# Optimization experiments

Measured on AMD Instinct MI355X. Metric: run time of the kernel, lower is better.

The kernel has to match this reference:

```python
import math
import jax, jax.numpy as jnp
import numpy as np

B, H, T, D = 4, 16, 1024, 64


def setup_inputs() -> dict:
    key0 = jax.random.key(0)
    ks = jax.random.split(key0, 5)
    return {
        "query": jax.random.normal(ks[0], (B, H, T, D), dtype=jnp.float32),
        "key": jax.random.normal(ks[1], (B, H, T, D), dtype=jnp.float32),
        "value": jax.random.normal(ks[2], (B, H, T, D), dtype=jnp.float32),
        "edges_key": jax.random.normal(ks[3], (T, T, D), dtype=jnp.float32),
        "edges_value": jax.random.normal(ks[4], (T, T, D), dtype=jnp.float32),
        "mask": jnp.ones((B, 1, 1, T), dtype=bool),
    }


def reference(query, key, value, edges_key, edges_value, mask):
    d = query.shape[-1]
    # content-content scores [B,H,T,T]
    scores = jnp.einsum("bhqd,bhkd->bhqk", query, key)
    # content-position scores via relative edge keys [T,T,D]
    scores = scores + jnp.einsum("bhqd,qkd->bhqk", query, edges_key)
    scores = scores * (1.0 / math.sqrt(d))
    scores = jnp.where(mask, scores, jnp.float32(-1e9))
    a = jax.nn.softmax(scores, axis=-1)  # dropout is identity in eval / pdrop=0
    # value update + relative edge-value update
    out = jnp.einsum("bhqk,bhkd->bhqd", a, value)
    out = out + jnp.einsum("bhqk,qkd->bhqd", a, edges_value)
    return out
```

## Files before the change

### kernel.cpp

```cpp
#include <hip/hip_runtime.h>

#define Tt 1024
#define Dh 64
#define BHn 64
#define SCALE 0.125f

typedef __attribute__((ext_vector_type(4))) float f32x4;
typedef __attribute__((ext_vector_type(8))) short bf16x8;

__device__ inline unsigned short f2bf(float x){
  unsigned u = __float_as_uint(x);
  unsigned r = (u + 0x7FFFu + ((u >> 16) & 1u)) >> 16;
  return (unsigned short)r;
}
__device__ inline float bf2f(unsigned short h){
  return __uint_as_float(((unsigned)h) << 16);
}
__device__ inline ushort4 pack4(float4 f){
  ushort4 u; u.x=f2bf(f.x); u.y=f2bf(f.y); u.z=f2bf(f.z); u.w=f2bf(f.w); return u;
}
__device__ inline bf16x8 pack8(float4 a, float4 b){
  bf16x8 r;
  r[0]=(short)f2bf(a.x); r[1]=(short)f2bf(a.y); r[2]=(short)f2bf(a.z); r[3]=(short)f2bf(a.w);
  r[4]=(short)f2bf(b.x); r[5]=(short)f2bf(b.y); r[6]=(short)f2bf(b.z); r[7]=(short)f2bf(b.w);
  return r;
}
__device__ inline f32x4 mfma16(bf16x8 a, bf16x8 b, f32x4 c){
  return __builtin_amdgcn_mfma_f32_16x16x32_bf16(a, b, c, 0, 0, 0);
}

__device__ inline void stage64x64(const float* __restrict__ g, unsigned short (*lds)[68], int tid){
  int r = tid >> 2, c = (tid & 3) * 16;
  const float4* g4 = (const float4*)(g + (size_t)r * 64 + c);
  float4 f0 = g4[0], f1 = g4[1], f2_ = g4[2], f3 = g4[3];
  ushort4* d4 = (ushort4*)&lds[r][c];
  d4[0]=pack4(f0); d4[1]=pack4(f1); d4[2]=pack4(f2_); d4[3]=pack4(f3);
}
__device__ inline void stage64x64T(const float* __restrict__ g, unsigned short (*lds)[68], int tid){
  int r = tid >> 2, c = (tid & 3) * 16;
  const float4* g4 = (const float4*)(g + (size_t)r * 64 + c);
  float4 f[4] = { g4[0], g4[1], g4[2], g4[3] };
#pragma unroll
  for (int i = 0; i < 4; ++i){
    lds[c + 4*i + 0][r] = f2bf(f[i].x);
    lds[c + 4*i + 1][r] = f2bf(f[i].y);
    lds[c + 4*i + 2][r] = f2bf(f[i].z);
    lds[c + 4*i + 3][r] = f2bf(f[i].w);
  }
}
__device__ inline void stage_rows(const unsigned short* __restrict__ g, size_t rowstride,
                                  unsigned short (*lds)[68], int tid){
  int r = tid >> 2, c = (tid & 3) * 16;
  const ushort4* s4 = (const ushort4*)(g + (size_t)r * rowstride + c);
  ushort4 u0=s4[0], u1=s4[1], u2=s4[2], u3=s4[3];
  ushort4* d4 = (ushort4*)&lds[r][c];
  d4[0]=u0; d4[1]=u1; d4[2]=u2; d4[3]=u3;
}
__device__ inline bf16x8 ldsfrag(const unsigned short (*lds)[68], int row, int col){
  const ushort4* p = (const ushort4*)&lds[row][col];
  ushort4 u0 = p[0], u1 = p[1];
  bf16x8 r;
  r[0]=(short)u0.x; r[1]=(short)u0.y; r[2]=(short)u0.z; r[3]=(short)u0.w;
  r[4]=(short)u1.x; r[5]=(short)u1.y; r[6]=(short)u1.z; r[7]=(short)u1.w;
  return r;
}
__device__ inline float fragsum(bf16x8 v){
  float s = 0.f;
#pragma unroll
  for (int i = 0; i < 8; ++i) s += bf2f((unsigned short)v[i]);
  return s;
}

__global__ __launch_bounds__(256) void k_qek(const float* __restrict__ Q,
                                             const float* __restrict__ EK,
                                             unsigned short* __restrict__ BIAS){
  __shared__ unsigned short ek[64][68];
  __shared__ unsigned short ot[64][68];
  const int qi = blockIdx.x;
  const int tid = threadIdx.x;
  const int w = tid >> 6, l = tid & 63, lr = l & 15, lg = l >> 4;

  bf16x8 a0, a1;
  {
    const int bh = 16*w + lr;
    const float4* q4 = (const float4*)(Q + ((size_t)bh * Tt + qi) * Dh);
    a0 = pack8(q4[lg*2],     q4[lg*2 + 1]);
    a1 = pack8(q4[8 + lg*2], q4[8 + lg*2 + 1]);
  }

  for (int kt = 0; kt < 16; ++kt){
    stage64x64(EK + ((size_t)qi * Tt + kt*64) * Dh, ek, tid);
    __syncthreads();
    f32x4 acc[4];
#pragma unroll
    for (int c = 0; c < 4; ++c){
      bf16x8 b0 = ldsfrag(ek, c*16 + lr, lg*8);
      bf16x8 b1 = ldsfrag(ek, c*16 + lr, lg*8 + 32);
      f32x4 z = {0.f,0.f,0.f,0.f};
      z = mfma16(a0, b0, z);
      z = mfma16(a1, b1, z);
      acc[c] = z;
    }
#pragma unroll
    for (int c = 0; c < 4; ++c)
#pragma unroll
      for (int j = 0; j < 4; ++j)
        ot[16*w + lg*4 + j][c*16 + lr] = f2bf(acc[c][j]);
    __syncthreads();
    {
      int r = tid >> 2, c2 = (tid & 3) * 16;
      unsigned short* dst = BIAS + (size_t)r * Tt * Tt + (size_t)qi * Tt + kt*64 + c2;
      const ushort4* s4 = (const ushort4*)&ot[r][c2];
      ushort4 u0=s4[0], u1=s4[1], u2=s4[2], u3=s4[3];
      ushort4* d4 = (ushort4*)dst;
      d4[0]=u0; d4[1]=u1; d4[2]=u2; d4[3]=u3;
    }
    __syncthreads();
  }
}

__global__ __launch_bounds__(256) void k_attn(const float* __restrict__ Q,
                                              const float* __restrict__ K,
                                              const float* __restrict__ V,
                                              unsigned short* __restrict__ WS,
                                              float* __restrict__ OUT){
  __shared__ unsigned short kt_[64][68];
  __shared__ unsigned short bt[64][68];
  __shared__ unsigned short pt[64][68];
  __shared__ unsigned short vt[64][68];
  const int qt = blockIdx.x * 64;
  const int bh = blockIdx.y;
  const int tid = threadIdx.x;
  const int w = tid >> 6, l = tid & 63, lr = l & 15, lg = l >> 4;

  bf16x8 a0, a1;
  {
    const float4* q4 = (const float4*)(Q + ((size_t)bh * Tt + qt + 16*w + lr) * Dh);
    a0 = pack8(q4[lg*2],     q4[lg*2 + 1]);
    a1 = pack8(q4[8 + lg*2], q4[8 + lg*2 + 1]);
  }

  float lsum[4] = {0.f, 0.f, 0.f, 0.f};
  f32x4 oacc[4];
#pragma unroll
  for (int c = 0; c < 4; ++c) oacc[c] = (f32x4){0.f,0.f,0.f,0.f};

  for (int kt = 0; kt < 16; ++kt){
    stage64x64(K + ((size_t)bh * Tt + kt*64) * Dh, kt_, tid);
    stage_rows(WS + (size_t)bh * Tt * Tt + (size_t)qt * Tt + kt*64, Tt, bt, tid);
    stage64x64T(V + ((size_t)bh * Tt + kt*64) * Dh, vt, tid);
    __syncthreads();
#pragma unroll
    for (int c = 0; c < 4; ++c){
      bf16x8 b0 = ldsfrag(kt_, c*16 + lr, lg*8);
      bf16x8 b1 = ldsfrag(kt_, c*16 + lr, lg*8 + 32);
      f32x4 z = {0.f,0.f,0.f,0.f};
      z = mfma16(a0, b0, z);
      z = mfma16(a1, b1, z);
      int kl = c*16 + lr;
#pragma unroll
      for (int j = 0; j < 4; ++j){
        float s = (z[j] + bf2f(bt[16*w + lg*4 + j][kl])) * SCALE;
        float p = __expf(s);
        lsum[j] += p;
        pt[16*w + lg*4 + j][kl] = f2bf(p);
      }
    }
    __syncthreads();
    {
      int r = tid >> 2, c2 = (tid & 3) * 16;
      unsigned short* dst = WS + (size_t)bh * Tt * Tt + (size_t)(qt + r) * Tt + kt*64 + c2;
      const ushort4* s4 = (const ushort4*)&pt[r][c2];
      ushort4 u0=s4[0], u1=s4[1], u2=s4[2], u3=s4[3];
      ushort4* d4 = (ushort4*)dst;
      d4[0]=u0; d4[1]=u1; d4[2]=u2; d4[3]=u3;
    }
    bf16x8 p0 = ldsfrag(pt, 16*w + lr, lg*8);
    bf16x8 p1 = ldsfrag(pt, 16*w + lr, lg*8 + 32);
#pragma unroll
    for (int c = 0; c < 4; ++c){
      bf16x8 v0 = ldsfrag(vt, c*16 + lr, lg*8);
      bf16x8 v1 = ldsfrag(vt, c*16 + lr, lg*8 + 32);
      oacc[c] = mfma16(p0, v0, oacc[c]);
      oacc[c] = mfma16(p1, v1, oacc[c]);
    }
    __syncthreads();
  }
  float rl[4];
#pragma unroll
  for (int j = 0; j < 4; ++j){
    float su = lsum[j];
    for (int o = 1; o < 16; o <<= 1) su += __shfl_xor(su, o, 64);
    rl[j] = 1.f / su;
  }
#pragma unroll
  for (int c = 0; c < 4; ++c)
#pragma unroll
    for (int j = 0; j < 4; ++j){
      int qrow = qt + 16*w + lg*4 + j;
      OUT[((size_t)bh * Tt + qrow) * Dh + c*16 + lr] = oacc[c][j] * rl[j];
    }
}

__global__ __launch_bounds__(256) void k_aev(const unsigned short* __restrict__ WS,
                                             const float* __restrict__ EV,
                                             float* __restrict__ OUT){
  __shared__ unsigned short at[64][68];
  __shared__ unsigned short evt[64][68];
  __shared__ float sums[64];
  const int qi = blockIdx.x;
  const int tid = threadIdx.x;
  const int w = tid >> 6, l = tid & 63, lr = l & 15, lg = l >> 4;

  f32x4 acc[4];
#pragma unroll
  for (int c = 0; c < 4; ++c) acc[c] = (f32x4){0.f,0.f,0.f,0.f};
  float asum = 0.f;

  for (int kt = 0; kt < 16; ++kt){
    stage_rows(WS + (size_t)qi * Tt + kt*64, (size_t)Tt * Tt, at, tid);
    stage64x64T(EV + ((size_t)qi * Tt + kt*64) * Dh, evt, tid);
    __syncthreads();
    bf16x8 a0 = ldsfrag(at, 16*w + lr, lg*8);
    bf16x8 a1 = ldsfrag(at, 16*w + lr, lg*8 + 32);
    asum += fragsum(a0) + fragsum(a1);
#pragma unroll
    for (int c = 0; c < 4; ++c){
      bf16x8 b0 = ldsfrag(evt, c*16 + lr, lg*8);
      bf16x8 b1 = ldsfrag(evt, c*16 + lr, lg*8 + 32);
      acc[c] = mfma16(a0, b0, acc[c]);
      acc[c] = mfma16(a1, b1, acc[c]);
    }
    __syncthreads();
  }
  asum += __shfl_xor(asum, 16, 64);
  asum += __shfl_xor(asum, 32, 64);
  if (lg == 0) sums[16*w + lr] = asum;
  __syncthreads();

#pragma unroll
  for (int c = 0; c < 4; ++c)
#pragma unroll
    for (int j = 0; j < 4; ++j){
      int bh = 16*w + lg*4 + j;
      float rl = 1.f / sums[bh];
      size_t idx = ((size_t)bh * Tt + qi) * Dh + c*16 + lr;
      OUT[idx] += acc[c][j] * rl;
    }
}

extern "C" void kernel_launch(void* const* d_in, const int* in_sizes, int n_in,
                              void* d_out, int out_size, void* d_ws, size_t ws_size,
                              hipStream_t stream){
  const float* Q  = (const float*)d_in[0];
  const float* K  = (const float*)d_in[1];
  const float* V  = (const float*)d_in[2];
  const float* EK = (const float*)d_in[3];
  const float* EV = (const float*)d_in[4];
  float* OUT = (float*)d_out;
  unsigned short* WS = (unsigned short*)d_ws;

  if (ws_size < (size_t)BHn * Tt * Tt * sizeof(unsigned short)) return;

  k_qek <<<dim3(1024),    dim3(256), 0, stream>>>(Q, EK, WS);
  k_attn<<<dim3(16, 64),  dim3(256), 0, stream>>>(Q, K, V, WS, OUT);
  k_aev <<<dim3(1024),    dim3(256), 0, stream>>>(WS, EV, OUT);
}
```

Measured before the change: 279.9 us.

## Drop LDS staging, load MFMA operands directly from global with wave-local sync

All three kernels stop staging K, V, EK, EV and bias tiles through shared memory. Each wave now loads its MFMA B-fragments straight from global memory, converting to bf16 in registers, and V/EV are read column-wise with strided scalar loads. Block-wide __syncthreads are replaced by wave barriers over per-wave LDS scratch. k_attn also moves to a flattened 1D grid whose index mapping groups heads for cache locality. The aim is to remove LDS traffic and block synchronisation, at the cost of redundant per-wave global loads and poorly coalesced column reads.

```diff
diff --git a/kernel.cpp b/kernel.cpp
--- a/kernel.cpp
+++ b/kernel.cpp
@@ -2,7 +2,6 @@
 
 #define Tt 1024
 #define Dh 64
-#define BHn 64
 #define SCALE 0.125f
 
 typedef __attribute__((ext_vector_type(4))) float f32x4;
@@ -15,9 +14,6 @@
 }
 __device__ inline float bf2f(unsigned short h){
   return __uint_as_float(((unsigned)h) << 16);
-}
-__device__ inline ushort4 pack4(float4 f){
-  ushort4 u; u.x=f2bf(f.x); u.y=f2bf(f.y); u.z=f2bf(f.z); u.w=f2bf(f.w); return u;
 }
 __device__ inline bf16x8 pack8(float4 a, float4 b){
   bf16x8 r;
@@ -28,33 +24,15 @@
 __device__ inline f32x4 mfma16(bf16x8 a, bf16x8 b, f32x4 c){
   return __builtin_amdgcn_mfma_f32_16x16x32_bf16(a, b, c, 0, 0, 0);
 }
-
-__device__ inline void stage64x64(const float* __restrict__ g, unsigned short (*lds)[68], int tid){
-  int r = tid >> 2, c = (tid & 3) * 16;
-  const float4* g4 = (const float4*)(g + (size_t)r * 64 + c);
-  float4 f0 = g4[0], f1 = g4[1], f2_ = g4[2], f3 = g4[3];
-  ushort4* d4 = (ushort4*)&lds[r][c];
-  d4[0]=pack4(f0); d4[1]=pack4(f1); d4[2]=pack4(f2_); d4[3]=pack4(f3);
-}
-__device__ inline void stage64x64T(const float* __restrict__ g, unsigned short (*lds)[68], int tid){
-  int r = tid >> 2, c = (tid & 3) * 16;
-  const float4* g4 = (const float4*)(g + (size_t)r * 64 + c);
-  float4 f[4] = { g4[0], g4[1], g4[2], g4[3] };
-#pragma unroll
-  for (int i = 0; i < 4; ++i){
-    lds[c + 4*i + 0][r] = f2bf(f[i].x);
-    lds[c + 4*i + 1][r] = f2bf(f[i].y);
-    lds[c + 4*i + 2][r] = f2bf(f[i].z);
-    lds[c + 4*i + 3][r] = f2bf(f[i].w);
-  }
-}
-__device__ inline void stage_rows(const unsigned short* __restrict__ g, size_t rowstride,
-                                  unsigned short (*lds)[68], int tid){
-  int r = tid >> 2, c = (tid & 3) * 16;
-  const ushort4* s4 = (const ushort4*)(g + (size_t)r * rowstride + c);
-  ushort4 u0=s4[0], u1=s4[1], u2=s4[2], u3=s4[3];
-  ushort4* d4 = (ushort4*)&lds[r][c];
-  d4[0]=u0; d4[1]=u1; d4[2]=u2; d4[3]=u3;
+__device__ inline bf16x8 loadB_row(const float* __restrict__ g, int row, int dlo){
+  const float4* p = (const float4*)(g + (size_t)row * Dh + dlo);
+  return pack8(p[0], p[1]);
+}
+__device__ inline bf16x8 loadB_col(const float* __restrict__ g, int klo, int d){
+  bf16x8 r;
+#pragma unroll
+  for (int i = 0; i < 8; ++i) r[i] = (short)f2bf(g[(size_t)(klo + i) * Dh + d]);
+  return r;
 }
 __device__ inline bf16x8 ldsfrag(const unsigned short (*lds)[68], int row, int col){
   const ushort4* p = (const ushort4*)&lds[row][col];
@@ -74,28 +52,28 @@
 __global__ __launch_bounds__(256) void k_qek(const float* __restrict__ Q,
                                              const float* __restrict__ EK,
                                              unsigned short* __restrict__ BIAS){
-  __shared__ unsigned short ek[64][68];
-  __shared__ unsigned short ot[64][68];
+  __shared__ unsigned short ot[4][16][68];
   const int qi = blockIdx.x;
   const int tid = threadIdx.x;
   const int w = tid >> 6, l = tid & 63, lr = l & 15, lg = l >> 4;
 
   bf16x8 a0, a1;
   {
-    const int bh = 16*w + lr;
-    const float4* q4 = (const float4*)(Q + ((size_t)bh * Tt + qi) * Dh);
+    const float4* q4 = (const float4*)(Q + ((size_t)(16*w + lr) * Tt + qi) * Dh);
     a0 = pack8(q4[lg*2],     q4[lg*2 + 1]);
     a1 = pack8(q4[8 + lg*2], q4[8 + lg*2 + 1]);
   }
+  const float* ekq = EK + (size_t)qi * Tt * Dh;
+  const int r = l >> 2, c2 = (l & 3) * 16;
+  unsigned short* dst0 = BIAS + (size_t)(16*w + r) * Tt * Tt + (size_t)qi * Tt + c2;
 
   for (int kt = 0; kt < 16; ++kt){
-    stage64x64(EK + ((size_t)qi * Tt + kt*64) * Dh, ek, tid);
-    __syncthreads();
+    const float* et = ekq + (size_t)kt * 64 * Dh;
     f32x4 acc[4];
 #pragma unroll
     for (int c = 0; c < 4; ++c){
-      bf16x8 b0 = ldsfrag(ek, c*16 + lr, lg*8);
-      bf16x8 b1 = ldsfrag(ek, c*16 + lr, lg*8 + 32);
+      bf16x8 b0 = loadB_row(et, c*16 + lr, lg*8);
+      bf16x8 b1 = loadB_row(et, c*16 + lr, lg*8 + 32);
       f32x4 z = {0.f,0.f,0.f,0.f};
       z = mfma16(a0, b0, z);
       z = mfma16(a1, b1, z);
@@ -105,31 +83,27 @@
     for (int c = 0; c < 4; ++c)
 #pragma unroll
       for (int j = 0; j < 4; ++j)
-        ot[16*w + lg*4 + j][c*16 + lr] = f2bf(acc[c][j]);
-    __syncthreads();
+        ot[w][lg*4 + j][c*16 + lr] = f2bf(acc[c][j]);
+    __builtin_amdgcn_wave_barrier();
     {
-      int r = tid >> 2, c2 = (tid & 3) * 16;
-      unsigned short* dst = BIAS + (size_t)r * Tt * Tt + (size_t)qi * Tt + kt*64 + c2;
-      const ushort4* s4 = (const ushort4*)&ot[r][c2];
+      const ushort4* s4 = (const ushort4*)&ot[w][r][c2];
       ushort4 u0=s4[0], u1=s4[1], u2=s4[2], u3=s4[3];
-      ushort4* d4 = (ushort4*)dst;
+      ushort4* d4 = (ushort4*)(dst0 + kt*64);
       d4[0]=u0; d4[1]=u1; d4[2]=u2; d4[3]=u3;
     }
-    __syncthreads();
+    __builtin_amdgcn_wave_barrier();
   }
 }
 
 __global__ __launch_bounds__(256) void k_attn(const float* __restrict__ Q,
                                               const float* __restrict__ K,
                                               const float* __restrict__ V,
-                                              unsigned short* __restrict__ WS,
+                                              unsigned short* WS,
                                               float* __restrict__ OUT){
-  __shared__ unsigned short kt_[64][68];
-  __shared__ unsigned short bt[64][68];
-  __shared__ unsigned short pt[64][68];
-  __shared__ unsigned short vt[64][68];
-  const int qt = blockIdx.x * 64;
-  const int bh = blockIdx.y;
+  __shared__ unsigned short pt[4][16][68];
+  const int bid = blockIdx.x;
+  const int bh = (bid & 7) + ((bid >> 7) << 3);
+  const int qt = ((bid >> 3) & 15) * 64;
   const int tid = threadIdx.x;
   const int w = tid >> 6, l = tid & 63, lr = l & 15, lg = l >> 4;
 
@@ -139,52 +113,53 @@
     a0 = pack8(q4[lg*2],     q4[lg*2 + 1]);
     a1 = pack8(q4[8 + lg*2], q4[8 + lg*2 + 1]);
   }
-
-  float lsum[4] = {0.f, 0.f, 0.f, 0.f};
+  const float* kb = K + (size_t)bh * Tt * Dh;
+  const float* vb = V + (size_t)bh * Tt * Dh;
+  unsigned short* wsb = WS + (size_t)bh * Tt * Tt;
+
+  float lsum[4] = {0.f,0.f,0.f,0.f};
   f32x4 oacc[4];
 #pragma unroll
   for (int c = 0; c < 4; ++c) oacc[c] = (f32x4){0.f,0.f,0.f,0.f};
 
+  const int r = l >> 2, c2 = (l & 3) * 16;
+
   for (int kt = 0; kt < 16; ++kt){
-    stage64x64(K + ((size_t)bh * Tt + kt*64) * Dh, kt_, tid);
-    stage_rows(WS + (size_t)bh * Tt * Tt + (size_t)qt * Tt + kt*64, Tt, bt, tid);
-    stage64x64T(V + ((size_t)bh * Tt + kt*64) * Dh, vt, tid);
-    __syncthreads();
-#pragma unroll
-    for (int c = 0; c < 4; ++c){
-      bf16x8 b0 = ldsfrag(kt_, c*16 + lr, lg*8);
-      bf16x8 b1 = ldsfrag(kt_, c*16 + lr, lg*8 + 32);
+    const float* ktl = kb + (size_t)kt * 64 * Dh;
+    const float* vtl = vb + (size_t)kt * 64 * Dh;
+#pragma unroll
+    for (int c = 0; c < 4; ++c){
+      const int kcol = c*16 + lr;
+      bf16x8 b0 = loadB_row(ktl, kcol, lg*8);
+      bf16x8 b1 = loadB_row(ktl, kcol, lg*8 + 32);
       f32x4 z = {0.f,0.f,0.f,0.f};
       z = mfma16(a0, b0, z);
       z = mfma16(a1, b1, z);
-      int kl = c*16 + lr;
 #pragma unroll
       for (int j = 0; j < 4; ++j){
-        float s = (z[j] + bf2f(bt[16*w + lg*4 + j][kl])) * SCALE;
-        float p = __expf(s);
+        float bias = bf2f(wsb[(size_t)(qt + 16*w + lg*4 + j) * Tt + kt*64 + kcol]);
+        float p = __expf((z[j] + bias) * SCALE);
         lsum[j] += p;
-        pt[16*w + lg*4 + j][kl] = f2bf(p);
+        pt[w][lg*4 + j][kcol] = f2bf(p);
       }
     }
-    __syncthreads();
+    __builtin_amdgcn_wave_barrier();
     {
-      int r = tid >> 2, c2 = (tid & 3) * 16;
-      unsigned short* dst = WS + (size_t)bh * Tt * Tt + (size_t)(qt + r) * Tt + kt*64 + c2;
-      const ushort4* s4 = (const ushort4*)&pt[r][c2];
+      const ushort4* s4 = (const ushort4*)&pt[w][r][c2];
       ushort4 u0=s4[0], u1=s4[1], u2=s4[2], u3=s4[3];
-      ushort4* d4 = (ushort4*)dst;
+      ushort4* d4 = (ushort4*)(wsb + (size_t)(qt + 16*w + r) * Tt + kt*64 + c2);
       d4[0]=u0; d4[1]=u1; d4[2]=u2; d4[3]=u3;
     }
-    bf16x8 p0 = ldsfrag(pt, 16*w + lr, lg*8);
-    bf16x8 p1 = ldsfrag(pt, 16*w + lr, lg*8 + 32);
-#pragma unroll
-    for (int c = 0; c < 4; ++c){
-      bf16x8 v0 = ldsfrag(vt, c*16 + lr, lg*8);
-      bf16x8 v1 = ldsfrag(vt, c*16 + lr, lg*8 + 32);
+    bf16x8 p0 = ldsfrag(pt[w], lr, lg*8);
+    bf16x8 p1 = ldsfrag(pt[w], lr, lg*8 + 32);
+#pragma unroll
+    for (int c = 0; c < 4; ++c){
+      bf16x8 v0 = loadB_col(vtl, lg*8,      c*16 + lr);
+      bf16x8 v1 = loadB_col(vtl, lg*8 + 32, c*16 + lr);
       oacc[c] = mfma16(p0, v0, oacc[c]);
       oacc[c] = mfma16(p1, v1, oacc[c]);
     }
-    __syncthreads();
+    __builtin_amdgcn_wave_barrier();
   }
   float rl[4];
 #pragma unroll
@@ -196,47 +171,43 @@
 #pragma unroll
   for (int c = 0; c < 4; ++c)
 #pragma unroll
-    for (int j = 0; j < 4; ++j){
-      int qrow = qt + 16*w + lg*4 + j;
-      OUT[((size_t)bh * Tt + qrow) * Dh + c*16 + lr] = oacc[c][j] * rl[j];
-    }
+    for (int j = 0; j < 4; ++j)
+      OUT[((size_t)bh * Tt + qt + 16*w + lg*4 + j) * Dh + c*16 + lr] = oacc[c][j] * rl[j];
 }
 
 __global__ __launch_bounds__(256) void k_aev(const unsigned short* __restrict__ WS,
                                              const float* __restrict__ EV,
                                              float* __restrict__ OUT){
-  __shared__ unsigned short at[64][68];
-  __shared__ unsigned short evt[64][68];
   __shared__ float sums[64];
   const int qi = blockIdx.x;
   const int tid = threadIdx.x;
   const int w = tid >> 6, l = tid & 63, lr = l & 15, lg = l >> 4;
 
+  const unsigned short* arow = WS + (size_t)(16*w + lr) * Tt * Tt + (size_t)qi * Tt;
+  const float* evq = EV + (size_t)qi * Tt * Dh;
+
   f32x4 acc[4];
 #pragma unroll
   for (int c = 0; c < 4; ++c) acc[c] = (f32x4){0.f,0.f,0.f,0.f};
   float asum = 0.f;
 
   for (int kt = 0; kt < 16; ++kt){
-    stage_rows(WS + (size_t)qi * Tt + kt*64, (size_t)Tt * Tt, at, tid);
-    stage64x64T(EV + ((size_t)qi * Tt + kt*64) * Dh, evt, tid);
-    __syncthreads();
-    bf16x8 a0 = ldsfrag(at, 16*w + lr, lg*8);
-    bf16x8 a1 = ldsfrag(at, 16*w + lr, lg*8 + 32);
+    bf16x8 a0 = *(const bf16x8*)(arow + kt*64 + lg*8);
+    bf16x8 a1 = *(const bf16x8*)(arow + kt*64 + 32 + lg*8);
     asum += fragsum(a0) + fragsum(a1);
-#pragma unroll
-    for (int c = 0; c < 4; ++c){
-      bf16x8 b0 = ldsfrag(evt, c*16 + lr, lg*8);
-      bf16x8 b1 = ldsfrag(evt, c*16 + lr, lg*8 + 32);
+    const float* evt = evq + (size_t)kt * 64 * Dh;
+#pragma unroll
+    for (int c = 0; c < 4; ++c){
+      bf16x8 b0 = loadB_col(evt, lg*8,      c*16 + lr);
+      bf16x8 b1 = loadB_col(evt, lg*8 + 32, c*16 + lr);
       acc[c] = mfma16(a0, b0, acc[c]);
       acc[c] = mfma16(a1, b1, acc[c]);
     }
-    __syncthreads();
   }
   asum += __shfl_xor(asum, 16, 64);
   asum += __shfl_xor(asum, 32, 64);
   if (lg == 0) sums[16*w + lr] = asum;
-  __syncthreads();
+  __builtin_amdgcn_wave_barrier();
 
 #pragma unroll
   for (int c = 0; c < 4; ++c)
@@ -260,9 +231,9 @@
   float* OUT = (float*)d_out;
   unsigned short* WS = (unsigned short*)d_ws;
 
-  if (ws_size < (size_t)BHn * Tt * Tt * sizeof(unsigned short)) return;
-
-  k_qek <<<dim3(1024),    dim3(256), 0, stream>>>(Q, EK, WS);
-  k_attn<<<dim3(16, 64),  dim3(256), 0, stream>>>(Q, K, V, WS, OUT);
-  k_aev <<<dim3(1024),    dim3(256), 0, stream>>>(WS, EV, OUT);
-}
+  if (ws_size < (size_t)64 * Tt * Tt * sizeof(unsigned short)) return;
+
+  k_qek <<<dim3(1024), dim3(256), 0, stream>>>(Q, EK, WS);
+  k_attn<<<dim3(1024), dim3(256), 0, stream>>>(Q, K, V, WS, OUT);
+  k_aev <<<dim3(1024), dim3(256), 0, stream>>>(WS, EV, OUT);
+}
```

After: 513.6 us. 83.5% more time.
